# Kernel tuning notes

Hardware: AMD Instinct MI355X
Metric: run time of the kernel (lower is better)

Reference implementation:

```python
import math
import jax, jax.numpy as jnp
import numpy as np

SR = 44100.0
N_SAMPLES = 65536
BW_OCT = 1.0
F0_HZ = 440.0            # f0_min_hz == f0_max_hz -> fixed, no RNG
AM_HZ_MIN, AM_HZ_MAX = 4.0, 16.0
FM_OCT_HZ_MIN, FM_OCT_HZ_MAX = 0.5, 4.0
SIGMA0 = 0.1
BW_N_SAMPLES = int(BW_OCT * SR)   # 44100
LN2 = math.log(2.0)


def setup_inputs() -> dict:
    key = jax.random.key(0)
    k1, k2, k3 = jax.random.split(key, 3)
    B = 256
    theta_am_hz_0to1 = jax.random.uniform(k1, (B,), dtype=jnp.float32)
    theta_fm_hz_0to1 = jax.random.uniform(k2, (B,), dtype=jnp.float32)
    seed = jax.random.randint(k3, (B,), 0, 100000).astype(jnp.int64)
    return {"theta_am_hz_0to1": theta_am_hz_0to1,
            "theta_fm_hz_0to1": theta_fm_hz_0to1,
            "seed": seed}


def _synth(theta_am_hz_0to1, theta_fm_hz_0to1):
    # map [0,1] -> log2-uniform in [min,max]
    am_lo, am_hi = math.log2(AM_HZ_MIN), math.log2(AM_HZ_MAX)
    fm_lo, fm_hi = math.log2(FM_OCT_HZ_MIN), math.log2(FM_OCT_HZ_MAX)
    am_hz = jnp.exp2(theta_am_hz_0to1 * (am_hi - am_lo) + am_lo)      # [B]
    fm_hz = jnp.exp2(theta_fm_hz_0to1 * (fm_hi - fm_lo) + fm_lo)      # [B]

    # time support and gaussian-window support (both [N])
    t = (jnp.arange(N_SAMPLES, dtype=jnp.float32) - N_SAMPLES // 2) / SR
    half = (N_SAMPLES - 1) / 2.0
    win_support = jnp.linspace(-half, half, N_SAMPLES, dtype=jnp.float32)

    fm = fm_hz[:, None]                                               # [B,1]
    am = am_hz[:, None]                                               # [B,1]
    two_pi = 2.0 * jnp.pi

    # FM chirp phase: f0/(fm*ln2) * (2^(fm*t) - 1)
    phi = (F0_HZ / (fm * LN2)) * (jnp.exp2(fm * t) - 1.0)             # [B,N]
    carrier = jnp.sin(two_pi * phi)
    modulator = jnp.sin(two_pi * am * 0.5 * t)

    # gaussian window, std = |sigma0 * bw_n_samples / fm| (per sample)
    window_std = jnp.abs(SIGMA0 * BW_N_SAMPLES / fm)                  # [B,1]
    w = win_support * (1.0 / (window_std * math.sqrt(2.0)))
    window = jnp.exp(-(w * w))                                        # [B,N]

    chirp = carrier * fm * window * modulator                         # fm!=0, am>0
    return chirp[:, None, :]                                          # [B,1,N]


def reference(theta_am_hz_0to1, theta_fm_hz_0to1, seed):
    # seed is unused: f0_min==f0_max and delta_min==delta_max==0, so the
    # per-sample torch RNG in the original is never consulted.
    return _synth(theta_am_hz_0to1, theta_fm_hz_0to1)
```

## Files before the change

### kernel.cpp

```cpp
#include <hip/hip_runtime.h>

#define N_SAMPLES 65536
#define CHUNKS_PER_BATCH 64

__global__ __launch_bounds__(256) void chirplet_synth_kernel(
    const float* __restrict__ theta_am,
    const float* __restrict__ theta_fm,
    float* __restrict__ out)
{
    const int bid   = blockIdx.x;
    const int b     = bid >> 6;
    const int chunk = bid & (CHUNKS_PER_BATCH - 1);
    const int n0    = (chunk << 10) + (threadIdx.x << 2);

    const float ta = theta_am[b];
    const float tf = theta_fm[b];
    const float am = exp2f(ta * 2.0f + 2.0f);
    const float fm = exp2f(tf * 3.0f - 1.0f);
    const float c        = 440.0f / (fm * 0.69314718055994531f);
    const float inv_den  = fm * (1.0f / (4410.0f * 1.41421356237309505f));
    const float am_half  = am * 0.5f;
    const float inv_sr   = 1.0f / 44100.0f;
    const float LOG2E    = 1.44269504088896340f;

    float4 r;
    float res[4];
#pragma unroll
    for (int i = 0; i < 4; ++i) {
        const float nf = (float)(n0 + i);
        const float t  = (nf - 32768.0f) * inv_sr;
        const float ws = nf - 32767.5f;

        const float e    = exp2f(fm * t);
        const float phi  = c * (e - 1.0f);
        const float carr = __builtin_amdgcn_sinf(__builtin_amdgcn_fractf(phi));

        const float mrev = am_half * t;
        const float modu = __builtin_amdgcn_sinf(__builtin_amdgcn_fractf(mrev));

        const float wv  = ws * inv_den;
        const float win = exp2f(-(wv * wv) * LOG2E);

        res[i] = carr * fm * win * modu;
    }
    r.x = res[0]; r.y = res[1]; r.z = res[2]; r.w = res[3];
    *reinterpret_cast<float4*>(&out[(size_t)b * N_SAMPLES + n0]) = r;
}

extern "C" void kernel_launch(void* const* d_in, const int* in_sizes, int n_in,
                              void* d_out, int out_size, void* d_ws, size_t ws_size,
                              hipStream_t stream) {
    const float* theta_am = (const float*)d_in[0];
    const float* theta_fm = (const float*)d_in[1];
    float* out = (float*)d_out;

    const int B = in_sizes[0];
    dim3 grid(B * CHUNKS_PER_BATCH), block(256);
    chirplet_synth_kernel<<<grid, block, 0, stream>>>(theta_am, theta_fm, out);
}
```

Baseline: 89.88 us.

## Skip Gaussian-negligible chunks and process larger chunks per block with nontemporal stores

Each block now covers 4096 samples instead of 1024, with each thread doing four strided float4 groups. Blocks whose whole chunk lies beyond a cutoff radius of the Gaussian window (about five normalized std units) write zeros without any transcendental math. Stores become nontemporal. The cutoff replaces tiny values (~1e-11 relative) with exact zeros, so it is a tolerance-based approximation, and it makes work per block uneven.

```diff
diff --git a/kernel.cpp b/kernel.cpp
--- a/kernel.cpp
+++ b/kernel.cpp
@@ -1,7 +1,10 @@
 #include <hip/hip_runtime.h>
 
-#define N_SAMPLES 65536
-#define CHUNKS_PER_BATCH 64
+#define NS 65536
+#define CHUNK_LOG 4
+#define CHUNK_SAMPLES 4096
+
+typedef float f32x4 __attribute__((ext_vector_type(4)));
 
 __global__ __launch_bounds__(256) void chirplet_synth_kernel(
     const float* __restrict__ theta_am,
@@ -9,42 +12,57 @@
     float* __restrict__ out)
 {
     const int bid   = blockIdx.x;
-    const int b     = bid >> 6;
-    const int chunk = bid & (CHUNKS_PER_BATCH - 1);
-    const int n0    = (chunk << 10) + (threadIdx.x << 2);
+    const int b     = bid >> CHUNK_LOG;
+    const int chunk = bid & ((1 << CHUNK_LOG) - 1);
+    const int base  = chunk * CHUNK_SAMPLES;
 
-    const float ta = theta_am[b];
     const float tf = theta_fm[b];
-    const float am = exp2f(ta * 2.0f + 2.0f);
     const float fm = exp2f(tf * 3.0f - 1.0f);
-    const float c        = 440.0f / (fm * 0.69314718055994531f);
-    const float inv_den  = fm * (1.0f / (4410.0f * 1.41421356237309505f));
-    const float am_half  = am * 0.5f;
-    const float inv_sr   = 1.0f / 44100.0f;
-    const float LOG2E    = 1.44269504088896340f;
 
-    float4 r;
-    float res[4];
+    float* outp = out + (size_t)b * NS + base + (threadIdx.x << 2);
+
+    const float T  = 31182.0f / fm;
+    const float lo = (float)base - 32767.5f;
+    const float hi = (float)(base + CHUNK_SAMPLES - 1) - 32767.5f;
+    if (lo > T || hi < -T) {
+        const f32x4 z = {0.f, 0.f, 0.f, 0.f};
 #pragma unroll
-    for (int i = 0; i < 4; ++i) {
-        const float nf = (float)(n0 + i);
-        const float t  = (nf - 32768.0f) * inv_sr;
-        const float ws = nf - 32767.5f;
+        for (int j = 0; j < 4; ++j)
+            __builtin_nontemporal_store(z, reinterpret_cast<f32x4*>(outp + (j << 10)));
+        return;
+    }
 
-        const float e    = exp2f(fm * t);
-        const float phi  = c * (e - 1.0f);
-        const float carr = __builtin_amdgcn_sinf(__builtin_amdgcn_fractf(phi));
+    const float ta      = theta_am[b];
+    const float am      = exp2f(ta * 2.0f + 2.0f);
+    const float c       = 440.0f / (fm * 0.69314718055994531f);
+    const float inv_den = fm * (1.0f / 6236.68503f);
+    const float am_half = am * 0.5f;
+    const float inv_sr  = 1.0f / 44100.0f;
+    const float LOG2E   = 1.44269504088896340f;
 
-        const float mrev = am_half * t;
-        const float modu = __builtin_amdgcn_sinf(__builtin_amdgcn_fractf(mrev));
+#pragma unroll
+    for (int j = 0; j < 4; ++j) {
+        const int n0 = base + (threadIdx.x << 2) + (j << 10);
+        float res[4];
+#pragma unroll
+        for (int i = 0; i < 4; ++i) {
+            const float nf = (float)(n0 + i);
+            const float t  = (nf - 32768.0f) * inv_sr;
+            const float ws = nf - 32767.5f;
 
-        const float wv  = ws * inv_den;
-        const float win = exp2f(-(wv * wv) * LOG2E);
+            const float e    = exp2f(fm * t);
+            const float phi  = c * (e - 1.0f);
+            const float carr = __builtin_amdgcn_sinf(__builtin_amdgcn_fractf(phi));
+            const float modu = __builtin_amdgcn_sinf(__builtin_amdgcn_fractf(am_half * t));
 
-        res[i] = carr * fm * win * modu;
+            const float wv  = ws * inv_den;
+            const float win = exp2f(-(wv * wv) * LOG2E);
+
+            res[i] = carr * fm * win * modu;
+        }
+        f32x4 r = {res[0], res[1], res[2], res[3]};
+        __builtin_nontemporal_store(r, reinterpret_cast<f32x4*>(outp + (j << 10)));
     }
-    r.x = res[0]; r.y = res[1]; r.z = res[2]; r.w = res[3];
-    *reinterpret_cast<float4*>(&out[(size_t)b * N_SAMPLES + n0]) = r;
 }
 
 extern "C" void kernel_launch(void* const* d_in, const int* in_sizes, int n_in,
@@ -55,6 +73,6 @@
     float* out = (float*)d_out;
 
     const int B = in_sizes[0];
-    dim3 grid(B * CHUNKS_PER_BATCH), block(256);
+    dim3 grid(B << CHUNK_LOG), block(256);
     chirplet_synth_kernel<<<grid, block, 0, stream>>>(theta_am, theta_fm, out);
 }
```

Result: faster. 88.04 us (-2.0%).

## Replace per-sample transcendentals with geometric and rotation recurrences, skip negligible window regions

Applied to the files above, without the earlier changes.

Each thread now produces 8 strided groups of 4 samples instead of one group. The exp2 of the chirp, the Gaussian window and the AM sine are advanced by multiplicative and rotation recurrences rather than recomputed per sample. Groups whose Gaussian window falls below a threshold get zero stores, and stores are nontemporal. This cuts per-sample transcendental work and launches fewer blocks. In exchange it accumulates recurrence rounding error, especially in the chirp phase, where the large multiplier cph amplifies small errors in e.

```diff
diff --git a/kernel.cpp b/kernel.cpp
--- a/kernel.cpp
+++ b/kernel.cpp
@@ -1,50 +1,90 @@
 #include <hip/hip_runtime.h>
 
-#define N_SAMPLES 65536
-#define CHUNKS_PER_BATCH 64
+#define NS 65536
+
+typedef float f32x4 __attribute__((ext_vector_type(4)));
 
 __global__ __launch_bounds__(256) void chirplet_synth_kernel(
     const float* __restrict__ theta_am,
     const float* __restrict__ theta_fm,
     float* __restrict__ out)
 {
-    const int bid   = blockIdx.x;
-    const int b     = bid >> 6;
-    const int chunk = bid & (CHUNKS_PER_BATCH - 1);
-    const int n0    = (chunk << 10) + (threadIdx.x << 2);
+    const int bid  = blockIdx.x;
+    const int b    = bid >> 3;
+    const int c    = bid & 7;
+    const int tid4 = threadIdx.x << 2;
 
+    const float tf = theta_fm[b];
     const float ta = theta_am[b];
-    const float tf = theta_fm[b];
+    const float fm = exp2f(tf * 3.0f - 1.0f);
     const float am = exp2f(ta * 2.0f + 2.0f);
-    const float fm = exp2f(tf * 3.0f - 1.0f);
-    const float c        = 440.0f / (fm * 0.69314718055994531f);
-    const float inv_den  = fm * (1.0f / (4410.0f * 1.41421356237309505f));
-    const float am_half  = am * 0.5f;
-    const float inv_sr   = 1.0f / 44100.0f;
-    const float LOG2E    = 1.44269504088896340f;
 
-    float4 r;
-    float res[4];
+    const float inv_sr = 1.0f / 44100.0f;
+    const float cph = 440.0f / (fm * 0.69314718055994531f);
+    const float r1  = exp2f(fm * inv_sr);
+    const float rG  = exp2f(fm * (8192.0f * inv_sr));
+
+    const float invd = fm * (1.0f / 6236.68503f);
+    const float k2   = invd * invd * 1.44269504f;
+    const float P1   = exp2f(-2.0f * k2);
+    const float PG   = exp2f(-16384.0f * k2);
+
+    const float m1  = am * (0.5f * inv_sr);
+    const float sd1 = __builtin_amdgcn_sinf(m1);
+    const float cd1 = __builtin_amdgcn_cosf(m1);
+    const float mG  = __builtin_amdgcn_fractf(m1 * 8192.0f);
+    const float sdG = __builtin_amdgcn_sinf(mG);
+    const float cdG = __builtin_amdgcn_cosf(mG);
+
+    const int   n0  = (c << 10) + tid4;
+    const float nf0 = (float)n0;
+    const float t0  = (nf0 - 32768.0f) * inv_sr;
+    const float ws0 = nf0 - 32767.5f;
+
+    float e  = exp2f(fm * t0);
+    float vv = exp2f(-k2 * (2.0f * ws0 + 1.0f));
+    const float th0 = __builtin_amdgcn_fractf(am * 0.5f * t0);
+    float s  = __builtin_amdgcn_sinf(th0);
+    float cn = __builtin_amdgcn_cosf(th0);
+
+    float* outp = out + (size_t)b * NS + n0;
+    const f32x4 z = {0.f, 0.f, 0.f, 0.f};
+
 #pragma unroll
-    for (int i = 0; i < 4; ++i) {
-        const float nf = (float)(n0 + i);
-        const float t  = (nf - 32768.0f) * inv_sr;
-        const float ws = nf - 32767.5f;
+    for (int gi = 0; gi < 8; ++gi) {
+        const float ws = ws0 + (float)(gi << 13);
+        const float q  = -k2 * ws * ws;
+        float* o = outp + (gi << 13);
 
-        const float e    = exp2f(fm * t);
-        const float phi  = c * (e - 1.0f);
-        const float carr = __builtin_amdgcn_sinf(__builtin_amdgcn_fractf(phi));
+        if (q > -36.5f) {
+            float le = e, lv = vv, ls = s, lc = cn;
+            float g  = fm * exp2f(q);
+            float res[4];
+#pragma unroll
+            for (int i = 0; i < 4; ++i) {
+                const float phi  = __builtin_fmaf(cph, le, -cph);
+                const float carr = __builtin_amdgcn_sinf(__builtin_amdgcn_fractf(phi));
+                res[i] = carr * g * ls;
+                if (i < 3) {
+                    le *= r1;
+                    g  *= lv;  lv *= P1;
+                    const float ns2 = __builtin_fmaf(ls, cd1,  lc * sd1);
+                    const float nc2 = __builtin_fmaf(lc, cd1, -ls * sd1);
+                    ls = ns2; lc = nc2;
+                }
+            }
+            f32x4 r = {res[0], res[1], res[2], res[3]};
+            __builtin_nontemporal_store(r, reinterpret_cast<f32x4*>(o));
+        } else {
+            __builtin_nontemporal_store(z, reinterpret_cast<f32x4*>(o));
+        }
 
-        const float mrev = am_half * t;
-        const float modu = __builtin_amdgcn_sinf(__builtin_amdgcn_fractf(mrev));
-
-        const float wv  = ws * inv_den;
-        const float win = exp2f(-(wv * wv) * LOG2E);
-
-        res[i] = carr * fm * win * modu;
+        e  *= rG;
+        vv *= PG;
+        const float ns2 = __builtin_fmaf(s, cdG,  cn * sdG);
+        const float nc2 = __builtin_fmaf(cn, cdG, -s * sdG);
+        s = ns2; cn = nc2;
     }
-    r.x = res[0]; r.y = res[1]; r.z = res[2]; r.w = res[3];
-    *reinterpret_cast<float4*>(&out[(size_t)b * N_SAMPLES + n0]) = r;
 }
 
 extern "C" void kernel_launch(void* const* d_in, const int* in_sizes, int n_in,
@@ -55,6 +95,6 @@
     float* out = (float*)d_out;
 
     const int B = in_sizes[0];
-    dim3 grid(B * CHUNKS_PER_BATCH), block(256);
+    dim3 grid(B << 3), block(256);
     chirplet_synth_kernel<<<grid, block, 0, stream>>>(theta_am, theta_fm, out);
 }
```

Result: faster. 79.57 us (-11.5%).
